# Kernel optimization log

Measured on AMD Instinct MI355X. Metric: run time of the kernel, lower is better.

The kernel has to match this reference:

```python
import jax, jax.numpy as jnp
import numpy as np
import math

E = 1024
H = 16
D = E // H  # 64
B, T, S = 4, 1024, 1024


def setup_inputs() -> dict:
    key = jax.random.key(0)
    ks = jax.random.split(key, 10)
    sd = 1.0 / math.sqrt(D)
    se = 1.0 / math.sqrt(E)
    return {
        "query": jax.random.normal(ks[0], (B, T, E), jnp.float32),
        "paragraph_encoding": jax.random.normal(ks[1], (S, E), jnp.float32),
        "Wq": jax.random.normal(ks[2], (D, D), jnp.float32) * sd,
        "bq": jax.random.normal(ks[3], (D,), jnp.float32) * sd,
        "Wk": jax.random.normal(ks[4], (D, D), jnp.float32) * sd,
        "bk": jax.random.normal(ks[5], (D,), jnp.float32) * sd,
        "Wv": jax.random.normal(ks[6], (D, D), jnp.float32) * sd,
        "bv": jax.random.normal(ks[7], (D,), jnp.float32) * sd,
        "Wout": jax.random.normal(ks[8], (E, E), jnp.float32) * se,
        "bout": jax.random.normal(ks[9], (E,), jnp.float32) * se,
    }


def reference(query, paragraph_encoding, Wq, bq, Wk, bk, Wv, bv, Wout, bout):
    b, t, _ = query.shape
    s = paragraph_encoding.shape[0]
    # [B, H, T, D]
    q = query.reshape(b, t, H, D).transpose(0, 2, 1, 3)
    # [H, S, D] -- key/value shared across batch
    p = paragraph_encoding.reshape(s, H, D).transpose(1, 0, 2)
    # per-head linear projections (torch Linear: x @ W.T + b)
    q = q @ Wq.T + bq
    k = p @ Wk.T + bk
    v = p @ Wv.T + bv
    # scores scaled by sqrt(embed_size), NOT head_dim (faithful to source)
    scores = jnp.einsum("bhtd,hsd->bhts", q, k) / math.sqrt(E)
    attn = jax.nn.softmax(scores, axis=-1)
    # (mask is None in this configuration; masking would occur AFTER softmax)
    context = jnp.einsum("bhts,hsd->bhtd", attn, v)
    context = context.transpose(0, 2, 1, 3).reshape(b, t, E)
    return context @ Wout.T + bout
```

## Files before the change

kernel.cpp:

```cpp
#include <hip/hip_runtime.h>


typedef __attribute__((ext_vector_type(8))) short short8v;
typedef __attribute__((ext_vector_type(4))) short short4v;
typedef __attribute__((ext_vector_type(4))) float float4v;

#define MFMA_BF16(A, B, C) __builtin_amdgcn_mfma_f32_16x16x32_bf16(A, B, C, 0, 0, 0)

#if __has_builtin(__builtin_amdgcn_exp2f)
#define EXP2F(x) __builtin_amdgcn_exp2f(x)
#else
#define EXP2F(x) exp2f(x)
#endif

#define QSCALE 0.045084220027780106f

__device__ __forceinline__ short f2bf(float f) {
  union { float f; unsigned u; } v; v.f = f;
  unsigned r = v.u + 0x7FFFu + ((v.u >> 16) & 1u);
  return (short)(r >> 16);
}

__global__ __launch_bounds__(256) void proj_qkv(
    const float* __restrict__ query, const float* __restrict__ para,
    const float* __restrict__ Wq, const float* __restrict__ bq,
    const float* __restrict__ Wk, const float* __restrict__ bk,
    const float* __restrict__ Wv, const float* __restrict__ bv,
    short* __restrict__ qs, short* __restrict__ kb, short* __restrict__ vt) {
  const int task = blockIdx.x * 4 + (threadIdx.x >> 6);
  const int lane = threadIdx.x & 63;
  const int g = lane >> 4, c = lane & 15;

  const float* W;
  const float* bias;
  const float* xrow;
  int type, h, tile, bh = 0;
  if (task < 4096) {
    type = 0; bh = task >> 6; tile = task & 63; h = bh & 15;
    xrow = query + ((bh >> 4) * 1024 + tile * 16 + c) * 1024 + h * 64;
    W = Wq; bias = bq;
  } else if (task < 5120) {
    int idx = task - 4096;
    type = 1; h = idx >> 6; tile = idx & 63;
    xrow = para + (tile * 16 + c) * 1024 + h * 64;
    W = Wk; bias = bk;
  } else {
    int idx = task - 5120;
    type = 2; h = idx >> 6; tile = idx & 63;
    xrow = para + (tile * 16 + c) * 1024 + h * 64;
    W = Wv; bias = bv;
  }

  short8v af[2];
#pragma unroll
  for (int kh = 0; kh < 2; ++kh) {
    const float* xp = xrow + kh * 32 + g * 8;
    float4v x0 = *(const float4v*)xp;
    float4v x1 = *(const float4v*)(xp + 4);
    af[kh] = (short8v){ f2bf(x0.x), f2bf(x0.y), f2bf(x0.z), f2bf(x0.w),
                        f2bf(x1.x), f2bf(x1.y), f2bf(x1.z), f2bf(x1.w) };
  }

#pragma unroll
  for (int dn = 0; dn < 4; ++dn) {
    float4v acc = (float4v){0.f, 0.f, 0.f, 0.f};
#pragma unroll
    for (int kh = 0; kh < 2; ++kh) {
      const float* wp = W + (dn * 16 + c) * 64 + kh * 32 + g * 8;
      float4v w0 = *(const float4v*)wp;
      float4v w1 = *(const float4v*)(wp + 4);
      short8v bfr = (short8v){ f2bf(w0.x), f2bf(w0.y), f2bf(w0.z), f2bf(w0.w),
                               f2bf(w1.x), f2bf(w1.y), f2bf(w1.z), f2bf(w1.w) };
      acc = MFMA_BF16(af[kh], bfr, acc);
    }
    const float bc = bias[dn * 16 + c];
    if (type == 0) {
#pragma unroll
      for (int r = 0; r < 4; ++r) {
        const int t = tile * 16 + 4 * g + r;
        qs[(bh * 1024 + t) * 64 + dn * 16 + c] = f2bf((acc[r] + bc) * QSCALE);
      }
    } else if (type == 1) {
#pragma unroll
      for (int r = 0; r < 4; ++r) {
        const int s = tile * 16 + 4 * g + r;
        kb[(h * 1024 + s) * 64 + dn * 16 + c] = f2bf(acc[r] + bc);
      }
    } else {
      short4v pk = (short4v){ f2bf(acc[0] + bc), f2bf(acc[1] + bc),
                              f2bf(acc[2] + bc), f2bf(acc[3] + bc) };
      *(short4v*)(vt + (h * 64 + dn * 16 + c) * 1024 + tile * 16 + 4 * g) = pk;
    }
  }
}

__global__ __launch_bounds__(256) void cvt_wout(const float* __restrict__ wsrc,
                                                short* __restrict__ wdst) {
  const int i = (blockIdx.x * 256 + threadIdx.x) * 8;
  float4v x0 = *(const float4v*)(wsrc + i);
  float4v x1 = *(const float4v*)(wsrc + i + 4);
  short8v v = (short8v){ f2bf(x0.x), f2bf(x0.y), f2bf(x0.z), f2bf(x0.w),
                         f2bf(x1.x), f2bf(x1.y), f2bf(x1.z), f2bf(x1.w) };
  *(short8v*)(wdst + i) = v;
}

__global__ __launch_bounds__(512, 4) void attn_fwd(
    const short* __restrict__ qs, const short* __restrict__ kb,
    const short* __restrict__ vt, short* __restrict__ ctx) {
  __shared__ __align__(16) short kv[2][4096];
  __shared__ __align__(16) short plds[8][16][40];
  const int w = threadIdx.x >> 6;
  const int lane = threadIdx.x & 63;
  const int g = lane >> 4, c = lane & 15;
  const int bh = blockIdx.x >> 3;
  const int b = bh >> 4, h = bh & 15;
  const int t0 = (blockIdx.x & 7) * 128 + w * 16;

  const char* kvsrc;
  int stepb;
  char* ldsdst;
  if (w < 4) {
    const int r = w * 8 + (lane >> 3);
    const int q = (lane & 7) ^ (lane >> 3);
    kvsrc = (const char*)(kb + h * 65536) + r * 128 + q * 16;
    stepb = 4096;
    ldsdst = (char*)&kv[0][0] + w * 1024 + lane * 16;
  } else {
    const int d = (w - 4) * 16 + (lane >> 2);
    const int q = (lane & 3) ^ ((lane >> 3) & 3);
    kvsrc = (const char*)(vt + h * 65536) + d * 2048 + q * 16;
    stepb = 64;
    ldsdst = (char*)&kv[0][0] + 4096 + (w - 4) * 1024 + lane * 16;
  }

  int koff[2][2];
#pragma unroll
  for (int sm = 0; sm < 2; ++sm)
#pragma unroll
    for (int kh = 0; kh < 2; ++kh)
      koff[sm][kh] = (sm * 16 + c) * 128 + (((kh * 4 + g) ^ (c & 7)) * 16);
  int voff[4];
#pragma unroll
  for (int nt = 0; nt < 4; ++nt)
    voff[nt] = 4096 + (nt * 16 + c) * 64 + ((g ^ ((c >> 1) & 3)) * 16);

  const short* qbase = qs + (bh * 1024 + t0) * 64;
  short8v qf[2];
#pragma unroll
  for (int kh = 0; kh < 2; ++kh)
    qf[kh] = *(const short8v*)(qbase + c * 64 + kh * 32 + g * 8);

  float4v cacc[4];
#pragma unroll
  for (int nt = 0; nt < 4; ++nt) cacc[nt] = (float4v){0.f, 0.f, 0.f, 0.f};
  float denp = 0.f;

  short8v stg = *(const short8v*)kvsrc;
  *(short8v*)ldsdst = stg;

  const char* kv0 = (const char*)&kv[0][0];
  for (int i = 0; i < 32; ++i) {
    __syncthreads();
    if (i < 31)
      stg = *(const short8v*)(kvsrc + (i + 1) * stepb);

    const char* kvb = kv0 + (i & 1) * 8192;
    short8v kf[2][2];
#pragma unroll
    for (int sm = 0; sm < 2; ++sm)
#pragma unroll
      for (int kh = 0; kh < 2; ++kh)
        kf[sm][kh] = *(const short8v*)(kvb + koff[sm][kh]);
    short8v vf[4];
#pragma unroll
    for (int nt = 0; nt < 4; ++nt)
      vf[nt] = *(const short8v*)(kvb + voff[nt]);

#pragma unroll
    for (int sm = 0; sm < 2; ++sm) {
      float4v z = (float4v){0.f, 0.f, 0.f, 0.f};
      z = MFMA_BF16(kf[sm][0], qf[0], z);
      z = MFMA_BF16(kf[sm][1], qf[1], z);
      const float p0 = EXP2F(z[0]);
      const float p1 = EXP2F(z[1]);
      const float p2 = EXP2F(z[2]);
      const float p3 = EXP2F(z[3]);
      denp += (p0 + p1) + (p2 + p3);
      short4v pk = (short4v){ f2bf(p0), f2bf(p1), f2bf(p2), f2bf(p3) };
      *(short4v*)&plds[w][c][sm * 16 + 4 * g] = pk;
    }

    asm volatile("" ::: "memory");

    short8v pa = *(const short8v*)&plds[w][c][g * 8];
#pragma unroll
    for (int nt = 0; nt < 4; ++nt)
      cacc[nt] = MFMA_BF16(pa, vf[nt], cacc[nt]);

    asm volatile("" ::: "memory");

    if (i < 31)
      *(short8v*)(ldsdst + ((i + 1) & 1) * 8192) = stg;
  }

  denp += __shfl_xor(denp, 16);
  denp += __shfl_xor(denp, 32);

  const int orow0 = b * 1024 + t0;
  float inv[4];
#pragma unroll
  for (int r = 0; r < 4; ++r)
    inv[r] = 1.0f / __shfl(denp, 4 * g + r);
#pragma unroll
  for (int nt = 0; nt < 4; ++nt)
#pragma unroll
    for (int r = 0; r < 4; ++r) {
      const int row = orow0 + 4 * g + r;
      ctx[row * 1024 + h * 64 + nt * 16 + c] = f2bf(cacc[nt][r] * inv[r]);
    }
}

__global__ __launch_bounds__(512, 4) void out_proj(
    const short* __restrict__ ctx, const short* __restrict__ wb,
    const float* __restrict__ bout, float* __restrict__ out) {
  __shared__ __align__(16) short ab[2][6144];
  const int w = threadIdx.x >> 6;
  const int lane = threadIdx.x & 63;
  const int g = lane >> 4, c = lane & 15;
  const int mblk = (blockIdx.x & 31) * 128;
  const int n0 = (blockIdx.x >> 5) * 64;

  const int srow = w * 16 + (lane >> 2);
  const int sq = (lane & 3) ^ ((lane >> 3) & 3);
  const char* asrc = (const char*)ctx + (mblk + srow) * 2048 + sq * 16;
  char* adst = (char*)&ab[0][0] + w * 1024 + lane * 16;
  const char* bsrc = (const char*)wb + (n0 + srow) * 2048 + sq * 16;
  char* bdst = (char*)&ab[0][0] + 8192 + w * 1024 + lane * 16;

  const int sw = (g ^ ((c >> 1) & 3)) * 16;
  const int aoff = (w * 16 + c) * 64 + sw;
  int boff[4];
#pragma unroll
  for (int nt = 0; nt < 4; ++nt)
    boff[nt] = 8192 + (nt * 16 + c) * 64 + sw;

  float4v acc[4];
#pragma unroll
  for (int nt = 0; nt < 4; ++nt) acc[nt] = (float4v){0.f, 0.f, 0.f, 0.f};

  short8v sa = *(const short8v*)asrc;
  short8v sb = (short8v){0, 0, 0, 0, 0, 0, 0, 0};
  if (w < 4) sb = *(const short8v*)bsrc;
  *(short8v*)adst = sa;
  if (w < 4) *(short8v*)bdst = sb;

  const char* ab0 = (const char*)&ab[0][0];
  for (int i = 0; i < 32; ++i) {
    __syncthreads();
    if (i < 31) {
      sa = *(const short8v*)(asrc + (i + 1) * 64);
      if (w < 4) sb = *(const short8v*)(bsrc + (i + 1) * 64);
    }
    const char* abb = ab0 + (i & 1) * 12288;
    short8v a = *(const short8v*)(abb + aoff);
    short8v bb[4];
#pragma unroll
    for (int nt = 0; nt < 4; ++nt)
      bb[nt] = *(const short8v*)(abb + boff[nt]);
#pragma unroll
    for (int nt = 0; nt < 4; ++nt)
      acc[nt] = MFMA_BF16(a, bb[nt], acc[nt]);
    if (i < 31) {
      *(short8v*)(adst + ((i + 1) & 1) * 12288) = sa;
      if (w < 4) *(short8v*)(bdst + ((i + 1) & 1) * 12288) = sb;
    }
  }

  float bs[4];
#pragma unroll
  for (int nt = 0; nt < 4; ++nt) bs[nt] = bout[n0 + nt * 16 + c];

  const int m0 = mblk + w * 16;
#pragma unroll
  for (int nt = 0; nt < 4; ++nt)
#pragma unroll
    for (int r = 0; r < 4; ++r)
      out[(m0 + 4 * g + r) * 1024 + n0 + nt * 16 + c] = acc[nt][r] + bs[nt];
}

extern "C" void kernel_launch(void* const* d_in, const int* in_sizes, int n_in,
                              void* d_out, int out_size, void* d_ws, size_t ws_size,
                              hipStream_t stream) {
  const float* query = (const float*)d_in[0];
  const float* para  = (const float*)d_in[1];
  const float* Wq = (const float*)d_in[2];
  const float* bq = (const float*)d_in[3];
  const float* Wk = (const float*)d_in[4];
  const float* bk = (const float*)d_in[5];
  const float* Wv = (const float*)d_in[6];
  const float* bv = (const float*)d_in[7];
  const float* Wout = (const float*)d_in[8];
  const float* bout = (const float*)d_in[9];
  float* out = (float*)d_out;

  char* ws = (char*)d_ws;
  short* qs  = (short*)(ws);
  short* kb  = (short*)(ws + (8u  << 20));
  short* vt  = (short*)(ws + (10u << 20));
  short* ctx = (short*)(ws + (12u << 20));
  short* wb  = (short*)(ws + (20u << 20));

  proj_qkv<<<dim3(1536), dim3(256), 0, stream>>>(query, para, Wq, bq, Wk, bk,
                                                 Wv, bv, qs, kb, vt);
  cvt_wout<<<dim3(512), dim3(256), 0, stream>>>(Wout, wb);
  attn_fwd<<<dim3(512), dim3(512), 0, stream>>>(qs, kb, vt, ctx);
  out_proj<<<dim3(512), dim3(512), 0, stream>>>(ctx, wb, bout, out);
}
```

Baseline: 71.43 us.

## Give each attention wave two query tiles and compute softmax denominator via MFMA

The attention kernel now runs 4 waves per block instead of 8, and each wave handles 32 query rows (two 16-row tiles), so every K/V fragment read from LDS is reused across two query tiles. All threads load both K and V staging chunks, which replaces the per-wave K/V role split. The softmax denominator is now accumulated by an extra MFMA against a vector of bf16 ones instead of scalar adds and cross-lane shuffles, so it sums the same bf16-rounded probabilities used for the context. Block-to-(batch,head) mapping is also reordered so consecutive blocks share time tiles across heads. The cost is higher register pressure per wave and fewer waves per block to hide latency.

```diff
diff --git a/kernel.cpp b/kernel.cpp
--- a/kernel.cpp
+++ b/kernel.cpp
@@ -104,34 +104,25 @@
   *(short8v*)(wdst + i) = v;
 }
 
-__global__ __launch_bounds__(512, 4) void attn_fwd(
+__global__ __launch_bounds__(256, 4) void attn_fwd(
     const short* __restrict__ qs, const short* __restrict__ kb,
     const short* __restrict__ vt, short* __restrict__ ctx) {
   __shared__ __align__(16) short kv[2][4096];
-  __shared__ __align__(16) short plds[8][16][40];
-  const int w = threadIdx.x >> 6;
-  const int lane = threadIdx.x & 63;
+  __shared__ __align__(16) short plds[4][2][16][40];
+  const int tid = threadIdx.x;
+  const int w = tid >> 6;
+  const int lane = tid & 63;
   const int g = lane >> 4, c = lane & 15;
-  const int bh = blockIdx.x >> 3;
+  const int bh = blockIdx.x & 63;
   const int b = bh >> 4, h = bh & 15;
-  const int t0 = (blockIdx.x & 7) * 128 + w * 16;
-
-  const char* kvsrc;
-  int stepb;
-  char* ldsdst;
-  if (w < 4) {
-    const int r = w * 8 + (lane >> 3);
-    const int q = (lane & 7) ^ (lane >> 3);
-    kvsrc = (const char*)(kb + h * 65536) + r * 128 + q * 16;
-    stepb = 4096;
-    ldsdst = (char*)&kv[0][0] + w * 1024 + lane * 16;
-  } else {
-    const int d = (w - 4) * 16 + (lane >> 2);
-    const int q = (lane & 3) ^ ((lane >> 3) & 3);
-    kvsrc = (const char*)(vt + h * 65536) + d * 2048 + q * 16;
-    stepb = 64;
-    ldsdst = (char*)&kv[0][0] + 4096 + (w - 4) * 1024 + lane * 16;
-  }
+  const int t0 = (blockIdx.x >> 6) * 128 + w * 32;
+
+  const int kr = tid >> 3, kq = (tid & 7) ^ (kr & 7);
+  const char* ksrc = (const char*)(kb + h * 65536) + kr * 128 + kq * 16;
+  const int vd = tid >> 2, vq = (tid & 3) ^ ((vd >> 1) & 3);
+  const char* vsrc = (const char*)(vt + h * 65536) + vd * 2048 + vq * 16;
+  char* kdst = (char*)&kv[0][0] + tid * 16;
+  char* vdst = (char*)&kv[0][0] + 4096 + tid * 16;
 
   int koff[2][2];
 #pragma unroll
@@ -145,24 +136,37 @@
     voff[nt] = 4096 + (nt * 16 + c) * 64 + ((g ^ ((c >> 1) & 3)) * 16);
 
   const short* qbase = qs + (bh * 1024 + t0) * 64;
-  short8v qf[2];
-#pragma unroll
-  for (int kh = 0; kh < 2; ++kh)
-    qf[kh] = *(const short8v*)(qbase + c * 64 + kh * 32 + g * 8);
-
-  float4v cacc[4];
-#pragma unroll
-  for (int nt = 0; nt < 4; ++nt) cacc[nt] = (float4v){0.f, 0.f, 0.f, 0.f};
-  float denp = 0.f;
-
-  short8v stg = *(const short8v*)kvsrc;
-  *(short8v*)ldsdst = stg;
+  short8v qf[2][2];
+#pragma unroll
+  for (int tn = 0; tn < 2; ++tn)
+#pragma unroll
+    for (int kh = 0; kh < 2; ++kh)
+      qf[tn][kh] = *(const short8v*)(qbase + (tn * 16 + c) * 64 + kh * 32 + g * 8);
+
+  float4v cacc[2][4];
+#pragma unroll
+  for (int tn = 0; tn < 2; ++tn)
+#pragma unroll
+    for (int nt = 0; nt < 4; ++nt)
+      cacc[tn][nt] = (float4v){0.f, 0.f, 0.f, 0.f};
+  float4v dacc[2];
+  dacc[0] = (float4v){0.f, 0.f, 0.f, 0.f};
+  dacc[1] = (float4v){0.f, 0.f, 0.f, 0.f};
+  const short obf = (short)0x3F80;
+  const short8v ones = (short8v){obf, obf, obf, obf, obf, obf, obf, obf};
+
+  short8v sk = *(const short8v*)ksrc;
+  short8v sv = *(const short8v*)vsrc;
+  *(short8v*)kdst = sk;
+  *(short8v*)vdst = sv;
 
   const char* kv0 = (const char*)&kv[0][0];
   for (int i = 0; i < 32; ++i) {
     __syncthreads();
-    if (i < 31)
-      stg = *(const short8v*)(kvsrc + (i + 1) * stepb);
+    if (i < 31) {
+      sk = *(const short8v*)(ksrc + (i + 1) * 4096);
+      sv = *(const short8v*)(vsrc + (i + 1) * 64);
+    }
 
     const char* kvb = kv0 + (i & 1) * 8192;
     short8v kf[2][2];
@@ -177,47 +181,57 @@
       vf[nt] = *(const short8v*)(kvb + voff[nt]);
 
 #pragma unroll
-    for (int sm = 0; sm < 2; ++sm) {
-      float4v z = (float4v){0.f, 0.f, 0.f, 0.f};
-      z = MFMA_BF16(kf[sm][0], qf[0], z);
-      z = MFMA_BF16(kf[sm][1], qf[1], z);
-      const float p0 = EXP2F(z[0]);
-      const float p1 = EXP2F(z[1]);
-      const float p2 = EXP2F(z[2]);
-      const float p3 = EXP2F(z[3]);
-      denp += (p0 + p1) + (p2 + p3);
-      short4v pk = (short4v){ f2bf(p0), f2bf(p1), f2bf(p2), f2bf(p3) };
-      *(short4v*)&plds[w][c][sm * 16 + 4 * g] = pk;
-    }
+    for (int sm = 0; sm < 2; ++sm)
+#pragma unroll
+      for (int tn = 0; tn < 2; ++tn) {
+        float4v z = (float4v){0.f, 0.f, 0.f, 0.f};
+        z = MFMA_BF16(kf[sm][0], qf[tn][0], z);
+        z = MFMA_BF16(kf[sm][1], qf[tn][1], z);
+        const float p0 = EXP2F(z[0]);
+        const float p1 = EXP2F(z[1]);
+        const float p2 = EXP2F(z[2]);
+        const float p3 = EXP2F(z[3]);
+        short4v pk = (short4v){ f2bf(p0), f2bf(p1), f2bf(p2), f2bf(p3) };
+        *(short4v*)&plds[w][tn][c][sm * 16 + 4 * g] = pk;
+      }
 
     asm volatile("" ::: "memory");
 
-    short8v pa = *(const short8v*)&plds[w][c][g * 8];
-#pragma unroll
-    for (int nt = 0; nt < 4; ++nt)
-      cacc[nt] = MFMA_BF16(pa, vf[nt], cacc[nt]);
+    short8v pa[2];
+#pragma unroll
+    for (int tn = 0; tn < 2; ++tn)
+      pa[tn] = *(const short8v*)&plds[w][tn][c][g * 8];
+
+#pragma unroll
+    for (int tn = 0; tn < 2; ++tn) {
+#pragma unroll
+      for (int nt = 0; nt < 4; ++nt)
+        cacc[tn][nt] = MFMA_BF16(pa[tn], vf[nt], cacc[tn][nt]);
+      dacc[tn] = MFMA_BF16(pa[tn], ones, dacc[tn]);
+    }
 
     asm volatile("" ::: "memory");
 
-    if (i < 31)
-      *(short8v*)(ldsdst + ((i + 1) & 1) * 8192) = stg;
-  }
-
-  denp += __shfl_xor(denp, 16);
-  denp += __shfl_xor(denp, 32);
+    if (i < 31) {
+      *(short8v*)(kdst + ((i + 1) & 1) * 8192) = sk;
+      *(short8v*)(vdst + ((i + 1) & 1) * 8192) = sv;
+    }
+  }
 
   const int orow0 = b * 1024 + t0;
-  float inv[4];
-#pragma unroll
-  for (int r = 0; r < 4; ++r)
-    inv[r] = 1.0f / __shfl(denp, 4 * g + r);
-#pragma unroll
-  for (int nt = 0; nt < 4; ++nt)
-#pragma unroll
-    for (int r = 0; r < 4; ++r) {
-      const int row = orow0 + 4 * g + r;
-      ctx[row * 1024 + h * 64 + nt * 16 + c] = f2bf(cacc[nt][r] * inv[r]);
-    }
+#pragma unroll
+  for (int tn = 0; tn < 2; ++tn) {
+    float inv[4];
+#pragma unroll
+    for (int r = 0; r < 4; ++r) inv[r] = 1.0f / dacc[tn][r];
+#pragma unroll
+    for (int nt = 0; nt < 4; ++nt)
+#pragma unroll
+      for (int r = 0; r < 4; ++r) {
+        const int row = orow0 + tn * 16 + 4 * g + r;
+        ctx[row * 1024 + h * 64 + nt * 16 + c] = f2bf(cacc[tn][nt][r] * inv[r]);
+      }
+  }
 }
 
 __global__ __launch_bounds__(512, 4) void out_proj(
@@ -313,6 +327,6 @@
   proj_qkv<<<dim3(1536), dim3(256), 0, stream>>>(query, para, Wq, bq, Wk, bk,
                                                  Wv, bv, qs, kb, vt);
   cvt_wout<<<dim3(512), dim3(256), 0, stream>>>(Wout, wb);
-  attn_fwd<<<dim3(512), dim3(512), 0, stream>>>(qs, kb, vt, ctx);
+  attn_fwd<<<dim3(512), dim3(256), 0, stream>>>(qs, kb, vt, ctx);
   out_proj<<<dim3(512), dim3(512), 0, stream>>>(ctx, wb, bout, out);
 }
```

New measurement: 71.19 us. About the same (-0.3%).
